# Kernel optimization log

Hardware: AMD Instinct MI355X
Metric: run time of the kernel (lower is better)

Reference implementation:

```python
import jax, jax.numpy as jnp
import numpy as np

N_RELS = 3
MAX_COMPS = 128
EMBED_DIM = 256
BATCH = 64
SEQ_LEN = 2048


def setup_inputs() -> dict:
    key = jax.random.key(0)
    k1, k2, k3 = jax.random.split(key, 3)
    embds = jax.random.normal(k1, (BATCH, SEQ_LEN, EMBED_DIM), dtype=jnp.float32)
    # sparse component-selection mask; p=0.04 -> ~82 components/sample (< MAX_COMPS-1)
    choice_mask = jax.random.bernoulli(k2, 0.04, (BATCH, SEQ_LEN)).astype(jnp.int32)
    # hk.Linear(n_rels*embed_dim, with_bias=False): W [embed_dim, n_rels*embed_dim]
    W = jax.random.normal(k3, (EMBED_DIM, N_RELS * EMBED_DIM), dtype=jnp.float32) / np.sqrt(EMBED_DIM).astype(np.float32)
    return {"embds": embds, "choice_mask": choice_mask, "W": W}


def _single(embds, mask, W):
    """One sample: gather selected embeddings, pad, project, pairwise relation scores.
    embds: [S, D], mask: [S] int, W: [D, D*R]. Returns [M, M, R]."""
    M, D, R = MAX_COMPS, EMBED_DIM, N_RELS
    # stable sort moves selected positions to the front, preserving order
    order = jnp.argsort(-mask)                      # [S]
    gathered = embds[order[: M - 1]]                # [M-1, D]
    n = jnp.minimum(jnp.sum(mask), M - 1)           # number of real components
    valid = jnp.arange(M - 1) < n                   # [M-1]
    comps = jnp.where(valid[:, None], gathered, jnp.zeros((), embds.dtype))
    # root component = row of ones (pad constant_values=1 at the front in the original)
    from_embds = jnp.concatenate([jnp.ones((1, D), embds.dtype), comps], axis=0)  # [M, D]
    to_embds = (from_embds @ W).reshape(M, D, R)    # [M, D, R]
    # jnp.dot([M,D], [M,D,R]) contracts D -> [M, M, R]
    log_energies = jnp.einsum('id,jdr->ijr', from_embds, to_embds)
    # no links FROM the root component (index 0)
    log_energies = log_energies.at[0].set(-jnp.inf)
    pad_mask = jnp.concatenate([jnp.ones((1,), bool), valid])   # [M]
    available = pad_mask[:, None] & pad_mask[None, :]           # [M, M]
    return jnp.where(available[:, :, None], log_energies, -jnp.inf)


def reference(embds, choice_mask, W):
    return jax.vmap(lambda e, m: _single(e, m, W))(embds, choice_mask)
```

## Files before the change

### kernel.cpp

```cpp
#include <hip/hip_runtime.h>
#include <math.h>

#define BATCH 64
#define SEQ   2048
#define DIM   256
#define NREL  3
#define MC    128
#define MV    127
#define NCOL  (DIM*NREL)
#define OUTC  (MC*NREL)

#define NEG_SENTINEL (-3.0e38f)

typedef __attribute__((ext_vector_type(8))) short short8;
typedef __attribute__((ext_vector_type(4))) float floatx4;
typedef __attribute__((ext_vector_type(8))) unsigned short us8;

__device__ __forceinline__ unsigned short f2bf(float f) {
  unsigned int u = __builtin_bit_cast(unsigned int, f);
  unsigned int r = u + 0x7FFFu + ((u >> 16) & 1u);
  return (unsigned short)(r >> 16);
}

__global__ __launch_bounds__(256) void k_prep(const int* __restrict__ mask,
                                              const float* __restrict__ embds,
                                              const float* __restrict__ W,
                                              unsigned short* __restrict__ fwb,
                                              unsigned short* __restrict__ Wt,
                                              int* __restrict__ n_ws) {
  int t = threadIdx.x;
  if (blockIdx.x < 24) {
    int idx = blockIdx.x * 256 + t;
    int nn = idx >> 3;
    int k0 = (idx & 7) * 32;
    unsigned short tmp[32];
#pragma unroll
    for (int e = 0; e < 32; e++) tmp[e] = f2bf(W[(size_t)(k0 + e) * NCOL + nn]);
#pragma unroll
    for (int q = 0; q < 4; q++)
      *(us8*)(Wt + (size_t)nn * DIM + k0 + q * 8) = *(us8*)&tmp[q * 8];
    return;
  }
  int b = blockIdx.x - 24;
  int lane = t & 63, wv = t >> 6;
  __shared__ int sel[MV];
  __shared__ int wsum[4];
  const int* m = mask + (size_t)b * SEQ;
  int base = t * 8;
  int vals[8];
  int c = 0;
#pragma unroll
  for (int k = 0; k < 8; k++) { vals[k] = m[base + k]; c += (vals[k] != 0); }
  int inc = c;
#pragma unroll
  for (int off = 1; off < 64; off <<= 1) {
    int o = __shfl_up(inc, off, 64);
    if (lane >= off) inc += o;
  }
  if (lane == 63) wsum[wv] = inc;
  __syncthreads();
  int wbase = 0;
#pragma unroll
  for (int w = 0; w < 4; w++) if (w < wv) wbase += wsum[w];
  int total = wsum[0] + wsum[1] + wsum[2] + wsum[3];
  int rank = wbase + inc - c;
#pragma unroll
  for (int k = 0; k < 8; k++) {
    if (vals[k]) { if (rank < MV) sel[rank] = base + k; rank++; }
  }
  int n = (total < MV) ? total : MV;
  if (t == 0) n_ws[b] = n;
  __syncthreads();
  int lane16 = t & 15;
#pragma unroll
  for (int p = 0; p < 8; p++) {
    int i = p * 16 + (t >> 4);
    float f[16];
    if (i == 0) {
#pragma unroll
      for (int e = 0; e < 16; e++) f[e] = 1.f;
    } else if (i - 1 < n) {
      const float* src = embds + ((size_t)b * SEQ + sel[i - 1]) * DIM + lane16 * 16;
#pragma unroll
      for (int q = 0; q < 4; q++) *(float4*)&f[q * 4] = *(const float4*)(src + q * 4);
    } else {
#pragma unroll
      for (int e = 0; e < 16; e++) f[e] = 0.f;
    }
    us8 o0, o1;
#pragma unroll
    for (int e = 0; e < 8; e++) { o0[e] = f2bf(f[e]); o1[e] = f2bf(f[8 + e]); }
    unsigned short* dst = fwb + ((size_t)b * MC + i) * DIM + lane16 * 16;
    *(us8*)(dst) = o0;
    *(us8*)(dst + 8) = o1;
  }
}

#define LDB 264
__global__ __launch_bounds__(256) void k_fused(const unsigned short* __restrict__ fwb,
                                               const unsigned short* __restrict__ Wt,
                                               const int* __restrict__ n_ws,
                                               float* __restrict__ out) {
  int b = blockIdx.y;
  int bc = blockIdx.x;
  int j0 = bc * 32, c0 = bc * 96;
  const unsigned short* A = fwb + (size_t)b * MC * DIM;
  __shared__ unsigned short Bs[96 * LDB];
  int t = threadIdx.x;
  int w = t >> 6, l = t & 63;
  int lm = l & 15, lk = (l >> 4) * 8, rb = (l >> 4) * 4;

  floatx4 acc1[2][12] = {};
#pragma unroll 2
  for (int k0 = 0; k0 < DIM; k0 += 32) {
    short8 af0 = *(const short8*)(A + (size_t)(j0 + lm) * DIM + k0 + lk);
    short8 af1 = *(const short8*)(A + (size_t)(j0 + 16 + lm) * DIM + k0 + lk);
#pragma unroll
    for (int ni = 0; ni < 12; ni++) {
      int n = w * 192 + ni * 16 + lm;
      short8 bf = *(const short8*)(Wt + (size_t)n * DIM + k0 + lk);
      acc1[0][ni] = __builtin_amdgcn_mfma_f32_16x16x32_bf16(af0, bf, acc1[0][ni], 0, 0, 0);
      acc1[1][ni] = __builtin_amdgcn_mfma_f32_16x16x32_bf16(af1, bf, acc1[1][ni], 0, 0, 0);
    }
  }
#pragma unroll
  for (int ni = 0; ni < 12; ni++) {
    int n = w * 192 + ni * 16 + lm;
    int dd = n / 3, r = n - dd * 3;
#pragma unroll
    for (int mi = 0; mi < 2; mi++)
#pragma unroll
      for (int reg = 0; reg < 4; reg++) {
        int jl = mi * 16 + rb + reg;
        Bs[(jl * 3 + r) * LDB + dd] = f2bf(acc1[mi][ni][reg]);
      }
  }
  __syncthreads();

  floatx4 acc[2][6] = {};
#pragma unroll 2
  for (int k0 = 0; k0 < DIM; k0 += 32) {
    short8 af[2], bf[6];
#pragma unroll
    for (int mi = 0; mi < 2; mi++)
      af[mi] = *(const short8*)(A + (size_t)(w * 32 + mi * 16 + lm) * DIM + k0 + lk);
#pragma unroll
    for (int ci = 0; ci < 6; ci++)
      bf[ci] = *(const short8*)&Bs[(ci * 16 + lm) * LDB + k0 + lk];
#pragma unroll
    for (int mi = 0; mi < 2; mi++)
#pragma unroll
      for (int ci = 0; ci < 6; ci++)
        acc[mi][ci] = __builtin_amdgcn_mfma_f32_16x16x32_bf16(af[mi], bf[ci], acc[mi][ci], 0, 0, 0);
  }
  int n = n_ws[b];
#pragma unroll
  for (int mi = 0; mi < 2; mi++)
#pragma unroll
    for (int ci = 0; ci < 6; ci++) {
      int cg = c0 + ci * 16 + lm;
      int j = cg / 3;
      bool vj = (j == 0) || (j <= n);
#pragma unroll
      for (int reg = 0; reg < 4; reg++) {
        int i = w * 32 + mi * 16 + rb + reg;
        bool vi = (i > 0) && (i <= n);
        out[(size_t)b * MC * OUTC + (size_t)i * OUTC + cg] =
            (vi && vj) ? acc[mi][ci][reg] : NEG_SENTINEL;
      }
    }
}

extern "C" void kernel_launch(void* const* d_in, const int* in_sizes, int n_in,
                              void* d_out, int out_size, void* d_ws, size_t ws_size,
                              hipStream_t stream) {
  const float* embds = (const float*)d_in[0];
  const int*   mask  = (const int*)d_in[1];
  const float* W     = (const float*)d_in[2];
  float* out = (float*)d_out;

  char* ws = (char*)d_ws;
  int* n_ws = (int*)(ws + 0);
  unsigned short* fwb = (unsigned short*)(ws + 65536);
  unsigned short* Wt  = (unsigned short*)(ws + 65536 + 4*1024*1024);

  k_prep <<<dim3(24 + BATCH), dim3(256), 0, stream>>>(mask, embds, W, fwb, Wt, n_ws);
  k_fused<<<dim3(4, BATCH),   dim3(256), 0, stream>>>(fwb, Wt, n_ws, out);
}
```

Measured before the change: 200.0 us.

## Split prep and fused kernels into finer blocks to raise grid occupancy

New measurement: 202.0 us. Within noise of the previous version (+1.0%).

```diff
diff --git a/kernel.cpp b/kernel.cpp
--- a/kernel.cpp
+++ b/kernel.cpp
@@ -41,7 +41,8 @@
       *(us8*)(Wt + (size_t)nn * DIM + k0 + q * 8) = *(us8*)&tmp[q * 8];
     return;
   }
-  int b = blockIdx.x - 24;
+  int g = blockIdx.x - 24;
+  int b = g >> 2, part = g & 3;
   int lane = t & 63, wv = t >> 6;
   __shared__ int sel[MV];
   __shared__ int wsum[4];
@@ -69,11 +70,12 @@
     if (vals[k]) { if (rank < MV) sel[rank] = base + k; rank++; }
   }
   int n = (total < MV) ? total : MV;
-  if (t == 0) n_ws[b] = n;
+  if (part == 0 && t == 0) n_ws[b] = n;
   __syncthreads();
   int lane16 = t & 15;
 #pragma unroll
-  for (int p = 0; p < 8; p++) {
+  for (int pp = 0; pp < 2; pp++) {
+    int p = part * 2 + pp;
     int i = p * 16 + (t >> 4);
     float f[16];
     if (i == 0) {
@@ -103,61 +105,57 @@
                                                float* __restrict__ out) {
   int b = blockIdx.y;
   int bc = blockIdx.x;
-  int j0 = bc * 32, c0 = bc * 96;
+  int j0 = bc * 16, c0 = bc * 48;
   const unsigned short* A = fwb + (size_t)b * MC * DIM;
-  __shared__ unsigned short Bs[96 * LDB];
+  __shared__ unsigned short Bs[48 * LDB];
   int t = threadIdx.x;
   int w = t >> 6, l = t & 63;
   int lm = l & 15, lk = (l >> 4) * 8, rb = (l >> 4) * 4;
 
-  floatx4 acc1[2][12] = {};
+  floatx4 acc1[12] = {};
 #pragma unroll 2
   for (int k0 = 0; k0 < DIM; k0 += 32) {
     short8 af0 = *(const short8*)(A + (size_t)(j0 + lm) * DIM + k0 + lk);
-    short8 af1 = *(const short8*)(A + (size_t)(j0 + 16 + lm) * DIM + k0 + lk);
 #pragma unroll
     for (int ni = 0; ni < 12; ni++) {
-      int n = w * 192 + ni * 16 + lm;
-      short8 bf = *(const short8*)(Wt + (size_t)n * DIM + k0 + lk);
-      acc1[0][ni] = __builtin_amdgcn_mfma_f32_16x16x32_bf16(af0, bf, acc1[0][ni], 0, 0, 0);
-      acc1[1][ni] = __builtin_amdgcn_mfma_f32_16x16x32_bf16(af1, bf, acc1[1][ni], 0, 0, 0);
+      int nn = w * 192 + ni * 16 + lm;
+      short8 bf = *(const short8*)(Wt + (size_t)nn * DIM + k0 + lk);
+      acc1[ni] = __builtin_amdgcn_mfma_f32_16x16x32_bf16(af0, bf, acc1[ni], 0, 0, 0);
     }
   }
 #pragma unroll
   for (int ni = 0; ni < 12; ni++) {
-    int n = w * 192 + ni * 16 + lm;
-    int dd = n / 3, r = n - dd * 3;
+    int nn = w * 192 + ni * 16 + lm;
+    int dd = nn / 3, r = nn - dd * 3;
 #pragma unroll
-    for (int mi = 0; mi < 2; mi++)
-#pragma unroll
-      for (int reg = 0; reg < 4; reg++) {
-        int jl = mi * 16 + rb + reg;
-        Bs[(jl * 3 + r) * LDB + dd] = f2bf(acc1[mi][ni][reg]);
-      }
+    for (int reg = 0; reg < 4; reg++) {
+      int jl = rb + reg;
+      Bs[(jl * 3 + r) * LDB + dd] = f2bf(acc1[ni][reg]);
+    }
   }
   __syncthreads();
 
-  floatx4 acc[2][6] = {};
+  floatx4 acc[2][3] = {};
 #pragma unroll 2
   for (int k0 = 0; k0 < DIM; k0 += 32) {
-    short8 af[2], bf[6];
+    short8 af[2], bf[3];
 #pragma unroll
     for (int mi = 0; mi < 2; mi++)
       af[mi] = *(const short8*)(A + (size_t)(w * 32 + mi * 16 + lm) * DIM + k0 + lk);
 #pragma unroll
-    for (int ci = 0; ci < 6; ci++)
+    for (int ci = 0; ci < 3; ci++)
       bf[ci] = *(const short8*)&Bs[(ci * 16 + lm) * LDB + k0 + lk];
 #pragma unroll
     for (int mi = 0; mi < 2; mi++)
 #pragma unroll
-      for (int ci = 0; ci < 6; ci++)
+      for (int ci = 0; ci < 3; ci++)
         acc[mi][ci] = __builtin_amdgcn_mfma_f32_16x16x32_bf16(af[mi], bf[ci], acc[mi][ci], 0, 0, 0);
   }
   int n = n_ws[b];
 #pragma unroll
   for (int mi = 0; mi < 2; mi++)
 #pragma unroll
-    for (int ci = 0; ci < 6; ci++) {
+    for (int ci = 0; ci < 3; ci++) {
       int cg = c0 + ci * 16 + lm;
       int j = cg / 3;
       bool vj = (j == 0) || (j <= n);
@@ -184,6 +182,6 @@
   unsigned short* fwb = (unsigned short*)(ws + 65536);
   unsigned short* Wt  = (unsigned short*)(ws + 65536 + 4*1024*1024);
 
-  k_prep <<<dim3(24 + BATCH), dim3(256), 0, stream>>>(mask, embds, W, fwb, Wt, n_ws);
-  k_fused<<<dim3(4, BATCH),   dim3(256), 0, stream>>>(fwb, Wt, n_ws, out);
+  k_prep <<<dim3(24 + 4 * BATCH), dim3(256), 0, stream>>>(mask, embds, W, fwb, Wt, n_ws);
+  k_fused<<<dim3(8, BATCH),       dim3(256), 0, stream>>>(fwb, Wt, n_ws, out);
 }
```
